# Kernel optimization log

Hardware: AMD Instinct MI355X
Metric: run time of the kernel (lower is better)

## Reference

```python
import jax, jax.numpy as jnp
import numpy as np

DIM = 128          # per-head dim P (== feature dim of x, y)
HEADS = 8
INNER = DIM * HEADS  # 1024
HIDDEN = int(DIM * 4.0)  # 512
EPS = 1e-5
LS_INIT = 1e-5


def _ln(x, w, b):
    mu = jnp.mean(x, axis=-1, keepdims=True)
    var = jnp.var(x, axis=-1, keepdims=True)
    return (x - mu) * jax.lax.rsqrt(var + EPS) * w + b


def setup_inputs() -> dict:
    key = jax.random.key(0)
    ks = jax.random.split(key, 10)
    B, N, M = 8, 1024, 1024
    s_in = 1.0 / np.sqrt(DIM)
    s_inner = 1.0 / np.sqrt(INNER)
    s_hid = 1.0 / np.sqrt(HIDDEN)
    return {
        "x": jax.random.normal(ks[0], (B, N, DIM), jnp.float32),
        "y": jax.random.normal(ks[1], (B, M, DIM), jnp.float32),
        "norm_x_w": jnp.ones((DIM,), jnp.float32),
        "norm_x_b": jnp.zeros((DIM,), jnp.float32),
        "norm_y_w": jnp.ones((DIM,), jnp.float32),
        "norm_y_b": jnp.zeros((DIM,), jnp.float32),
        "q_w": jax.random.uniform(ks[2], (INNER, DIM), jnp.float32, -s_in, s_in),
        "kv_w": jax.random.uniform(ks[3], (2 * INNER, DIM), jnp.float32, -s_in, s_in),
        "proj_w": jax.random.uniform(ks[4], (DIM, INNER), jnp.float32, -s_inner, s_inner),
        "proj_b": jax.random.uniform(ks[5], (DIM,), jnp.float32, -s_inner, s_inner),
        "ls1_gamma": jnp.full((DIM,), LS_INIT, jnp.float32),
        "norm_out_w": jnp.ones((DIM,), jnp.float32),
        "norm_out_b": jnp.zeros((DIM,), jnp.float32),
        "fc1_w": jax.random.uniform(ks[6], (HIDDEN, DIM), jnp.float32, -s_in, s_in),
        "fc1_b": jax.random.uniform(ks[7], (HIDDEN,), jnp.float32, -s_in, s_in),
        "fc2_w": jax.random.uniform(ks[8], (DIM, HIDDEN), jnp.float32, -s_hid, s_hid),
        "fc2_b": jax.random.uniform(ks[9], (DIM,), jnp.float32, -s_hid, s_hid),
        "ls2_gamma": jnp.full((DIM,), LS_INIT, jnp.float32),
    }


def reference(x, y, norm_x_w, norm_x_b, norm_y_w, norm_y_b, q_w, kv_w,
              proj_w, proj_b, ls1_gamma, norm_out_w, norm_out_b,
              fc1_w, fc1_b, fc2_w, fc2_b, ls2_gamma):
    B, N, P = x.shape
    M = y.shape[1]
    scale = P ** (-0.5)

    xn = _ln(x, norm_x_w, norm_x_b)
    yn = _ln(y, norm_y_w, norm_y_b)

    # q: (B,N,H,P) -> bhnp ; kv: (B,M,2,H,P)
    q = (xn @ q_w.T).reshape(B, N, HEADS, P).transpose(0, 2, 1, 3)
    kv = (yn @ kv_w.T).reshape(B, M, 2, HEADS, P)
    k = kv[:, :, 0].transpose(0, 2, 1, 3)  # bhmp
    v = kv[:, :, 1].transpose(0, 2, 1, 3)  # bhmp

    attn = jnp.einsum('bhnp,bhmp->bhnm', q, k) * scale
    attn = jax.nn.softmax(attn, axis=-1)
    o = jnp.einsum('bhnm,bhmp->bhnp', attn, v)
    o = o.transpose(0, 2, 1, 3).reshape(B, N, INNER)
    o = o @ proj_w.T + proj_b
    x = x + o * ls1_gamma

    h = _ln(x, norm_out_w, norm_out_b)
    h = jax.nn.relu(h @ fc1_w.T + fc1_b)
    h = h @ fc2_w.T + fc2_b
    x = x + h * ls2_gamma
    return x
```

## Files before the change

kernel.cpp:

```cpp
#include <hip/hip_runtime.h>
#include <stdint.h>

#define DIM    128
#define HEADS  8
#define INNER  1024
#define HIDDEN 512
#define BATCH  8
#define SEQ    1024
#define ROWS   8192

typedef __attribute__((ext_vector_type(8))) short bf16x8;
typedef __attribute__((ext_vector_type(4))) float f32x4;
typedef __attribute__((ext_vector_type(4))) unsigned short u16x4;

#define QSCALE (0.08838834764831845f * 1.4426950408889634f)

#define AS1 __attribute__((address_space(1)))
#define AS3 __attribute__((address_space(3)))

static __device__ __forceinline__ float b2f(unsigned short u) {
    union { float f; unsigned int i; } v; v.i = ((unsigned int)u) << 16; return v.f;
}
static __device__ __forceinline__ unsigned short f2b(float f) {
    union { float f; unsigned int i; } v; v.f = f;
    unsigned int x = v.i;
    return (unsigned short)((x + 0x7fffu + ((x >> 16) & 1u)) >> 16);
}
static __device__ __forceinline__ unsigned int cvt_pk_bf16(float a, float b) {
    unsigned int r;
    asm("v_cvt_pk_bf16_f32 %0, %1, %2" : "=v"(r) : "v"(a), "v"(b));
    return r;
}
static __device__ __forceinline__ void gl_lds16(const unsigned short* g, unsigned short* l) {
    __builtin_amdgcn_global_load_lds((AS1 void*)g, (AS3 void*)l, 16, 0, 0);
}

static __device__ __forceinline__ size_t pa_idx(int row, int k, int K) {
    return ((size_t)((row >> 4) * (K >> 5) + (k >> 5)) << 9)
         + (size_t)(((((k >> 3) & 3) << 4) + (row & 15)) << 3) + (size_t)(k & 7);
}

template<int K>
static __device__ __forceinline__ void cvtw(const float* __restrict__ W,
                                            unsigned short* __restrict__ Wp, int j)
{
    const int c  = j & 15;
    const int gw = (j >> 4) & 3;
    const int blk = j >> 6;
    const int ks = blk & ((K >> 5) - 1);
    const int nt = blk / (K >> 5);
    const int n  = nt * 16 + c;
    const int kb = ks * 32 + gw * 8;
    const float4 a = *(const float4*)(W + (size_t)n * K + kb);
    const float4 b = *(const float4*)(W + (size_t)n * K + kb + 4);
    u16x4 o0, o1;
    o0[0] = f2b(a.x); o0[1] = f2b(a.y); o0[2] = f2b(a.z); o0[3] = f2b(a.w);
    o1[0] = f2b(b.x); o1[1] = f2b(b.y); o1[2] = f2b(b.z); o1[3] = f2b(b.w);
    *(u16x4*)(Wp + (size_t)j * 8)     = o0;
    *(u16x4*)(Wp + (size_t)j * 8 + 4) = o1;
}

__global__ __launch_bounds__(256)
void cvt_all_kernel(const float* __restrict__ s0, unsigned short* __restrict__ d0,
                    const float* __restrict__ s1, unsigned short* __restrict__ d1,
                    const float* __restrict__ s2, unsigned short* __restrict__ d2,
                    const float* __restrict__ s3, unsigned short* __restrict__ d3,
                    const float* __restrict__ s4, unsigned short* __restrict__ d4)
{
    int j = blockIdx.x * 256 + threadIdx.x;
    if (j < 16384)                 { cvtw<128>(s0, d0, j);  return; }
    if ((j -= 16384) < 32768)      { cvtw<128>(s1, d1, j);  return; }
    if ((j -= 32768) < 16384)      { cvtw<1024>(s2, d2, j); return; }
    if ((j -= 16384) < 8192)       { cvtw<128>(s3, d3, j);  return; }
    j -= 8192;                       cvtw<512>(s4, d4, j);
}

static __device__ __forceinline__ void ln_row(const float* __restrict__ in,
                                              const float* __restrict__ w,
                                              const float* __restrict__ b,
                                              unsigned short* __restrict__ out,
                                              int row, int lane)
{
    const float2 xv = *(const float2*)(in + (size_t)row*DIM + lane*2);
    float x0 = xv.x, x1 = xv.y;
    float s = x0 + x1;
    float q = x0*x0 + x1*x1;
    #pragma unroll
    for (int off = 32; off > 0; off >>= 1) {
        s += __shfl_xor(s, off);
        q += __shfl_xor(q, off);
    }
    const float mu  = s * (1.0f/128.0f);
    const float var = q * (1.0f/128.0f) - mu*mu;
    const float rs  = rsqrtf(var + 1e-5f);
    const float2 wv = *(const float2*)(w + lane*2);
    const float2 bv = *(const float2*)(b + lane*2);
    unsigned short o0 = f2b((x0 - mu) * rs * wv.x + bv.x);
    unsigned short o1 = f2b((x1 - mu) * rs * wv.y + bv.y);
    *(unsigned int*)(out + pa_idx(row, lane*2, 128)) = (unsigned int)o0 | ((unsigned int)o1 << 16);
}

__global__ __launch_bounds__(256)
void ln_dual_kernel(const float* __restrict__ inx, const float* __restrict__ wx,
                    const float* __restrict__ bx, unsigned short* __restrict__ outx,
                    const float* __restrict__ iny, const float* __restrict__ wy,
                    const float* __restrict__ by, unsigned short* __restrict__ outy)
{
    const int row  = blockIdx.x * 4 + (threadIdx.x >> 6);
    const int lane = threadIdx.x & 63;
    if (blockIdx.y == 0) ln_row(inx, wx, bx, outx, row, lane);
    else                 ln_row(iny, wy, by, outy, row, lane);
}

__global__ __launch_bounds__(256)
void qkv_kernel(const unsigned short* __restrict__ xn,
                const unsigned short* __restrict__ yn,
                const unsigned short* __restrict__ wq,
                const unsigned short* __restrict__ wkv,
                unsigned short* __restrict__ qb,
                unsigned short* __restrict__ kpm,
                unsigned short* __restrict__ vpm)
{
    const int lane = threadIdx.x & 63;
    const int wave = threadIdx.x >> 6;
    const int g    = lane >> 4;
    const int c16  = lane & 15;
    const int bx   = blockIdx.x;
    const int by   = blockIdx.y;

    f32x4 acc[4];
    #pragma unroll
    for (int t = 0; t < 4; ++t) acc[t] = (f32x4){0.f, 0.f, 0.f, 0.f};

    if (bx < 32) {
        const bool isq = bx < 16;
        const unsigned short* W = isq ? wq : wkv;
        const unsigned short* Aact = isq ? xn : yn;
        const int wt = (bx & 15) * 4 + wave;
        #pragma unroll
        for (int ks = 0; ks < 4; ++ks) {
            bf16x8 wf = *(const bf16x8*)(W + (((size_t)(wt*4 + ks)) << 9) + lane*8);
            #pragma unroll
            for (int t = 0; t < 4; ++t) {
                bf16x8 af = *(const bf16x8*)(Aact + (((size_t)((by*4 + t)*4 + ks)) << 9) + lane*8);
                acc[t] = __builtin_amdgcn_mfma_f32_16x16x32_bf16(wf, af, acc[t], 0, 0, 0);
            }
        }
        const int n_w0 = (bx & 15)*64 + wave*16 + g*4;
        const int hh = n_w0 >> 7;
        const int p0 = n_w0 & 127;
        #pragma unroll
        for (int t = 0; t < 4; ++t) {
            const int m_row = by*64 + t*16 + c16;
            const int bb = m_row >> 10, m = m_row & 1023;
            u16x4 o;
            if (isq) {
                o[0] = f2b(acc[t][0]*QSCALE); o[1] = f2b(acc[t][1]*QSCALE);
                o[2] = f2b(acc[t][2]*QSCALE); o[3] = f2b(acc[t][3]*QSCALE);
                *(u16x4*)&qb[(((size_t)(bb*HEADS + hh))*SEQ + m)*DIM + p0] = o;
            } else {
                o[0] = f2b(acc[t][0]); o[1] = f2b(acc[t][1]);
                o[2] = f2b(acc[t][2]); o[3] = f2b(acc[t][3]);
                const int chunk = m >> 5, sl = (m >> 4) & 1, cl = m & 15;
                const int ksl = p0 >> 5, gl = (p0 >> 3) & 3, el0 = p0 & 7;
                *(u16x4*)&kpm[(size_t)(bb*HEADS + hh)*SEQ*DIM
                    + (size_t)((chunk*8 + sl*4 + ksl)*64 + gl*16 + cl)*8 + el0] = o;
            }
        }
    } else {
        const int mt = by*4 + wave;
        #pragma unroll
        for (int ks = 0; ks < 4; ++ks) {
            bf16x8 af = *(const bf16x8*)(yn + (((size_t)(mt*4 + ks)) << 9) + lane*8);
            #pragma unroll
            for (int t = 0; t < 4; ++t) {
                const int nt = 64 + (bx - 32)*4 + t;
                bf16x8 wf = *(const bf16x8*)(wkv + (((size_t)(nt*4 + ks)) << 9) + lane*8);
                acc[t] = __builtin_amdgcn_mfma_f32_16x16x32_bf16(af, wf, acc[t], 0, 0, 0);
            }
        }
        const int m_row0 = by*64 + wave*16 + g*4;
        const int bb = m_row0 >> 10;
        const int m0 = m_row0 & 1023;
        const int chunk = m0 >> 5, gl = (m0 >> 3) & 3, el0 = m0 & 7;
        #pragma unroll
        for (int t = 0; t < 4; ++t) {
            const int p = (bx - 32)*64 + t*16 + c16;
            const int hh = p >> 7, pp = p & 127, pcl = pp >> 4, cl = pp & 15;
            u16x4 o;
            o[0] = f2b(acc[t][0]); o[1] = f2b(acc[t][1]);
            o[2] = f2b(acc[t][2]); o[3] = f2b(acc[t][3]);
            *(u16x4*)&vpm[(size_t)(bb*HEADS + hh)*SEQ*DIM
                + (size_t)((chunk*8 + pcl)*64 + gl*16 + cl)*8 + el0] = o;
        }
    }
}

__global__ __launch_bounds__(512)
void attn_kernel(const unsigned short* __restrict__ qbuf,
                 const unsigned short* __restrict__ kperm,
                 const unsigned short* __restrict__ vperm,
                 unsigned short* __restrict__ obuf)
{
    __shared__ unsigned short kbuf[2][8192];
    __shared__ unsigned short vbuf[2][8192];
    __shared__ unsigned short pls[8][640];

    const int lane = threadIdx.x & 63;
    const int wave = threadIdx.x >> 6;
    const int g    = lane >> 4;
    const int c16  = lane & 15;

    const int j    = blockIdx.x;
    const int bh   = (j & 7) * 8 + (j >> 6);
    const int nblk = (j >> 3) & 7;
    const int n0   = nblk * 128 + wave * 16;
    const int bb   = bh >> 3, hh = bh & 7;

    const unsigned short* Q  = qbuf  + (size_t)bh * SEQ * DIM;
    const unsigned short* Kb = kperm + (size_t)bh * SEQ * DIM;
    const unsigned short* Vb = vperm + (size_t)bh * SEQ * DIM;

    #pragma unroll
    for (int i = 0; i < 4; ++i) {
        gl_lds16(Kb + (wave*4 + i)*512 + lane*8, &kbuf[0][(wave*4 + i)*512]);
        gl_lds16(Vb + (wave*4 + i)*512 + lane*8, &vbuf[0][(wave*4 + i)*512]);
    }

    bf16x8 qf[4];
    #pragma unroll
    for (int ks = 0; ks < 4; ++ks)
        qf[ks] = *(const bf16x8*)(Q + (size_t)(n0 + c16)*DIM + ks*32 + g*8);

    f32x4 oacc[8];
    #pragma unroll
    for (int pc = 0; pc < 8; ++pc) oacc[pc] = (f32x4){0.f,0.f,0.f,0.f};
    float mi = 8.0f;
    float li0 = 0.f, li1 = 0.f;

    __syncthreads();

    int cur = 0;
    for (int ip = 0; ip < 16; ++ip, cur ^= 1) {
        if (ip != 15) {
            const unsigned short* Ks = Kb + (size_t)(ip + 1) * 8192;
            const unsigned short* Vs = Vb + (size_t)(ip + 1) * 8192;
            #pragma unroll
            for (int i = 0; i < 4; ++i) {
                gl_lds16(Ks + (wave*4 + i)*512 + lane*8, &kbuf[cur ^ 1][(wave*4 + i)*512]);
                gl_lds16(Vs + (wave*4 + i)*512 + lane*8, &vbuf[cur ^ 1][(wave*4 + i)*512]);
            }
        }

        f32x4 st[4];
        #pragma unroll
        for (int c = 0; c < 2; ++c)
            #pragma unroll
            for (int s = 0; s < 2; ++s) {
                f32x4 a = (f32x4){0.f,0.f,0.f,0.f};
                #pragma unroll
                for (int ks = 0; ks < 4; ++ks) {
                    bf16x8 kf = *(const bf16x8*)&kbuf[cur][c*4096 + (s*4 + ks)*512 + lane*8];
                    a = __builtin_amdgcn_mfma_f32_16x16x32_bf16(kf, qf[ks], a, 0, 0, 0);
                }
                st[c*2 + s] = a;
            }

        #pragma unroll
        for (int c = 0; c < 2; ++c) {
            bf16x8 vf[8];
            #pragma unroll
            for (int pc = 0; pc < 8; ++pc)
                vf[pc] = *(const bf16x8*)&vbuf[cur][c*4096 + (pc*64 + lane)*8];

            const f32x4 sa = st[c*2 + 0];
            const f32x4 sb = st[c*2 + 1];
            float cmax = fmaxf(fmaxf(fmaxf(sa[0], sa[1]), fmaxf(sa[2], sa[3])),
                               fmaxf(fmaxf(sb[0], sb[1]), fmaxf(sb[2], sb[3])));

            if (!__all(cmax - mi <= 8.0f)) {
                float rmax = cmax;
                rmax = fmaxf(rmax, __shfl_xor(rmax, 16));
                rmax = fmaxf(rmax, __shfl_xor(rmax, 32));
                const float mnew  = fmaxf(mi, rmax);
                const float alpha = exp2f(mi - mnew);
                mi = mnew;
                li0 *= alpha; li1 *= alpha;
                float ar[4];
                #pragma unroll
                for (int r = 0; r < 4; ++r) ar[r] = __shfl(alpha, g*4 + r);
                #pragma unroll
                for (int pc = 0; pc < 8; ++pc)
                    #pragma unroll
                    for (int r = 0; r < 4; ++r) oacc[pc][r] *= ar[r];
            }

            uint2 pw[2];
            {
                float p0 = exp2f(sa[0] - mi), p1 = exp2f(sa[1] - mi);
                float p2 = exp2f(sa[2] - mi), p3 = exp2f(sa[3] - mi);
                float p4 = exp2f(sb[0] - mi), p5 = exp2f(sb[1] - mi);
                float p6 = exp2f(sb[2] - mi), p7 = exp2f(sb[3] - mi);
                li0 += (p0 + p1) + (p2 + p3);
                li1 += (p4 + p5) + (p6 + p7);
                pw[0].x = cvt_pk_bf16(p0, p1); pw[0].y = cvt_pk_bf16(p2, p3);
                pw[1].x = cvt_pk_bf16(p4, p5); pw[1].y = cvt_pk_bf16(p6, p7);
            }

            unsigned short* pbase = &pls[wave][0];
            *(uint2*)(pbase + c16*40 + 0*16 + g*4) = pw[0];
            *(uint2*)(pbase + c16*40 + 1*16 + g*4) = pw[1];

            bf16x8 pa = *(const bf16x8*)(pbase + c16*40 + g*8);
            #pragma unroll
            for (int pc = 0; pc < 8; ++pc)
                oacc[pc] = __builtin_amdgcn_mfma_f32_16x16x32_bf16(pa, vf[pc], oacc[pc], 0, 0, 0);
        }

        __syncthreads();
    }

    float li = li0 + li1;
    li += __shfl_xor(li, 16);
    li += __shfl_xor(li, 32);
    float lr[4];
    #pragma unroll
    for (int r = 0; r < 4; ++r) lr[r] = 1.f / __shfl(li, g*4 + r);
    #pragma unroll
    for (int pc = 0; pc < 8; ++pc)
        #pragma unroll
        for (int r = 0; r < 4; ++r) {
            const int row = bb*SEQ + n0 + g*4 + r;
            const int k   = hh*DIM + pc*16 + c16;
            obuf[pa_idx(row, k, INNER)] = f2b(oacc[pc][r] * lr[r]);
        }
}

__global__ __launch_bounds__(256)
void projln_kernel(const unsigned short* __restrict__ A,
                   const unsigned short* __restrict__ W,
                   const float* __restrict__ bias,
                   const float* __restrict__ gamma,
                   const float* __restrict__ xres,
                   float* __restrict__ x1,
                   const float* __restrict__ lnw, const float* __restrict__ lnb,
                   unsigned short* __restrict__ hin)
{
    __shared__ float part[4][16][2];

    const int lane = threadIdx.x & 63;
    const int wave = threadIdx.x >> 6;
    const int g    = lane >> 4;
    const int c16  = lane & 15;
    const int mt   = blockIdx.x;

    f32x4 acc[2];
    acc[0] = (f32x4){0.f,0.f,0.f,0.f};
    acc[1] = (f32x4){0.f,0.f,0.f,0.f};

    #pragma unroll 4
    for (int ks = 0; ks < 32; ++ks) {
        bf16x8 af = *(const bf16x8*)(A + (((size_t)(mt*32 + ks)) << 9) + lane*8);
        #pragma unroll
        for (int t = 0; t < 2; ++t) {
            bf16x8 wf = *(const bf16x8*)(W + (((size_t)((wave*2 + t)*32 + ks)) << 9) + lane*8);
            acc[t] = __builtin_amdgcn_mfma_f32_16x16x32_bf16(af, wf, acc[t], 0, 0, 0);
        }
    }

    float v[2][4];
    #pragma unroll
    for (int t = 0; t < 2; ++t) {
        const int col = wave*32 + t*16 + c16;
        const float bb = bias[col], gg = gamma[col];
        #pragma unroll
        for (int r = 0; r < 4; ++r) {
            const int row = mt*16 + g*4 + r;
            const float xv = xres[(size_t)row*DIM + col];
            v[t][r] = xv + (acc[t][r] + bb) * gg;
            x1[(size_t)row*DIM + col] = v[t][r];
        }
    }
    #pragma unroll
    for (int r = 0; r < 4; ++r) {
        float s = v[0][r] + v[1][r];
        float q = v[0][r]*v[0][r] + v[1][r]*v[1][r];
        #pragma unroll
        for (int off = 1; off < 16; off <<= 1) {
            s += __shfl_xor(s, off);
            q += __shfl_xor(q, off);
        }
        if (c16 == 0) { part[wave][g*4+r][0] = s; part[wave][g*4+r][1] = q; }
    }
    __syncthreads();

    #pragma unroll
    for (int r = 0; r < 4; ++r) {
        const int lr = g*4 + r;
        const float s = part[0][lr][0] + part[1][lr][0] + part[2][lr][0] + part[3][lr][0];
        const float q = part[0][lr][1] + part[1][lr][1] + part[2][lr][1] + part[3][lr][1];
        const float mu  = s * (1.0f/128.0f);
        const float var = q * (1.0f/128.0f) - mu*mu;
        const float rs  = rsqrtf(var + 1e-5f);
        const int row = mt*16 + lr;
        #pragma unroll
        for (int t = 0; t < 2; ++t) {
            const int col = wave*32 + t*16 + c16;
            const float hv = (v[t][r] - mu) * rs * lnw[col] + lnb[col];
            hin[pa_idx(row, col, 128)] = f2b(hv);
        }
    }
}

__global__ __launch_bounds__(256)
void fc_kernel(const unsigned short* __restrict__ hin,
               const unsigned short* __restrict__ W1,
               const float* __restrict__ b1,
               const unsigned short* __restrict__ W2,
               const float* __restrict__ b2,
               const float* __restrict__ gamma2,
               const float* __restrict__ x1,
               float* __restrict__ dout)
{
    __shared__ unsigned short h[16][520];

    const int lane = threadIdx.x & 63;
    const int wave = threadIdx.x >> 6;
    const int g    = lane >> 4;
    const int c16  = lane & 15;
    const int mt   = blockIdx.x;

    f32x4 a1[8];
    #pragma unroll
    for (int t = 0; t < 8; ++t) a1[t] = (f32x4){0.f,0.f,0.f,0.f};
    #pragma unroll
    for (int ks = 0; ks < 4; ++ks) {
        bf16x8 af = *(const bf16x8*)(hin + (((size_t)(mt*4 + ks)) << 9) + lane*8);
        #pragma unroll
        for (int t = 0; t < 8; ++t) {
            const int nt = wave*8 + t;
            bf16x8 wf = *(const bf16x8*)(W1 + (((size_t)(nt*4 + ks)) << 9) + lane*8);
            a1[t] = __builtin_amdgcn_mfma_f32_16x16x32_bf16(af, wf, a1[t], 0, 0, 0);
        }
    }
    #pragma unroll
    for (int t = 0; t < 8; ++t) {
        const int col = wave*128 + t*16 + c16;
        const float bb = b1[col];
        #pragma unroll
        for (int r = 0; r < 4; ++r)
            h[g*4 + r][col] = f2b(fmaxf(a1[t][r] + bb, 0.f));
    }
    __syncthreads();

    f32x4 a2[2];
    a2[0] = (f32x4){0.f,0.f,0.f,0.f};
    a2[1] = (f32x4){0.f,0.f,0.f,0.f};
    #pragma unroll 4
    for (int ks = 0; ks < 16; ++ks) {
        bf16x8 af = *(const bf16x8*)&h[c16][ks*32 + g*8];
        #pragma unroll
        for (int t = 0; t < 2; ++t) {
            const int nt = wave*2 + t;
            bf16x8 wf = *(const bf16x8*)(W2 + (((size_t)(nt*16 + ks)) << 9) + lane*8);
            a2[t] = __builtin_amdgcn_mfma_f32_16x16x32_bf16(af, wf, a2[t], 0, 0, 0);
        }
    }
    #pragma unroll
    for (int t = 0; t < 2; ++t) {
        const int col = wave*32 + t*16 + c16;
        const float bb = b2[col], gg = gamma2[col];
        #pragma unroll
        for (int r = 0; r < 4; ++r) {
            const int row = mt*16 + g*4 + r;
            dout[(size_t)row*DIM + col] = x1[(size_t)row*DIM + col] + (a2[t][r] + bb) * gg;
        }
    }
}

extern "C" void kernel_launch(void* const* d_in, const int* in_sizes, int n_in,
                              void* d_out, int out_size, void* d_ws, size_t ws_size,
                              hipStream_t stream)
{
    const float* x         = (const float*)d_in[0];
    const float* y         = (const float*)d_in[1];
    const float* norm_x_w  = (const float*)d_in[2];
    const float* norm_x_b  = (const float*)d_in[3];
    const float* norm_y_w  = (const float*)d_in[4];
    const float* norm_y_b  = (const float*)d_in[5];
    const float* q_w       = (const float*)d_in[6];
    const float* kv_w      = (const float*)d_in[7];
    const float* proj_w    = (const float*)d_in[8];
    const float* proj_b    = (const float*)d_in[9];
    const float* ls1_gamma = (const float*)d_in[10];
    const float* norm_o_w  = (const float*)d_in[11];
    const float* norm_o_b  = (const float*)d_in[12];
    const float* fc1_w     = (const float*)d_in[13];
    const float* fc1_b     = (const float*)d_in[14];
    const float* fc2_w     = (const float*)d_in[15];
    const float* fc2_b     = (const float*)d_in[16];
    const float* ls2_gamma = (const float*)d_in[17];

    char* ws = (char*)d_ws;
    size_t off = 0;
    auto alloc = [&](size_t bytes) {
        void* p = ws + off;
        off += (bytes + 255) & ~(size_t)255;
        return p;
    };
    unsigned short* xn  = (unsigned short*)alloc((size_t)ROWS*DIM*2);
    unsigned short* yn  = (unsigned short*)alloc((size_t)ROWS*DIM*2);
    unsigned short* qb  = (unsigned short*)alloc((size_t)ROWS*INNER*2);
    unsigned short* kpm = (unsigned short*)alloc((size_t)ROWS*INNER*2);
    unsigned short* vpm = (unsigned short*)alloc((size_t)ROWS*INNER*2);
    unsigned short* ob  = (unsigned short*)alloc((size_t)ROWS*INNER*2);
    float*          x1  = (float*)alloc((size_t)ROWS*DIM*4);
    unsigned short* hin = (unsigned short*)alloc((size_t)ROWS*DIM*2);
    unsigned short* wq   = (unsigned short*)alloc((size_t)INNER*DIM*2);
    unsigned short* wkv  = (unsigned short*)alloc((size_t)2*INNER*DIM*2);
    unsigned short* wpr  = (unsigned short*)alloc((size_t)DIM*INNER*2);
    unsigned short* wf1  = (unsigned short*)alloc((size_t)HIDDEN*DIM*2);
    unsigned short* wf2  = (unsigned short*)alloc((size_t)DIM*HIDDEN*2);

    cvt_all_kernel<<<dim3(320), 256, 0, stream>>>(
        q_w, wq, kv_w, wkv, proj_w, wpr, fc1_w, wf1, fc2_w, wf2);

    ln_dual_kernel<<<dim3(ROWS/4, 2), 256, 0, stream>>>(
        x, norm_x_w, norm_x_b, xn, y, norm_y_w, norm_y_b, yn);

    qkv_kernel<<<dim3(48, ROWS/64), 256, 0, stream>>>(xn, yn, wq, wkv, qb, kpm, vpm);

    attn_kernel<<<dim3(512), 512, 0, stream>>>(qb, kpm, vpm, ob);

    projln_kernel<<<dim3(ROWS/16), 256, 0, stream>>>(
        ob, wpr, proj_b, ls1_gamma, x, x1, norm_o_w, norm_o_b, hin);

    fc_kernel<<<dim3(ROWS/16), 256, 0, stream>>>(
        hin, wf1, fc1_b, wf2, fc2_b, ls2_gamma, x1, (float*)d_out);
}
```

Baseline: 112.6 us.

## Switch attention to 32x32x16 MFMA tiles with register-shuffled P operand

The attention kernel now uses 32x32x16 bf16 MFMA instead of 16x16x32. It runs 4 waves per block, each owning 32 query rows, and processes 32 keys per iteration. The K/V permuted layouts written by the QKV kernel are rearranged to match the new operand fragments. The softmax probabilities are rearranged into the PV A-operand with cross-half lane shuffles rather than a round trip through LDS, which removes the per-wave P scratch buffer. The cost is more iterations with a block-wide barrier each, and more accumulator registers per wave.

```diff
diff --git a/kernel.cpp b/kernel.cpp
--- a/kernel.cpp
+++ b/kernel.cpp
@@ -11,6 +11,7 @@
 
 typedef __attribute__((ext_vector_type(8))) short bf16x8;
 typedef __attribute__((ext_vector_type(4))) float f32x4;
+typedef __attribute__((ext_vector_type(16))) float f32x16;
 typedef __attribute__((ext_vector_type(4))) unsigned short u16x4;
 
 #define QSCALE (0.08838834764831845f * 1.4426950408889634f)
@@ -161,10 +162,10 @@
             } else {
                 o[0] = f2b(acc[t][0]); o[1] = f2b(acc[t][1]);
                 o[2] = f2b(acc[t][2]); o[3] = f2b(acc[t][3]);
-                const int chunk = m >> 5, sl = (m >> 4) & 1, cl = m & 15;
-                const int ksl = p0 >> 5, gl = (p0 >> 3) & 3, el0 = p0 & 7;
+                const int chunk = m >> 5;
+                const int ds = p0 >> 4, dhi = (p0 >> 3) & 1, de = p0 & 7;
                 *(u16x4*)&kpm[(size_t)(bb*HEADS + hh)*SEQ*DIM
-                    + (size_t)((chunk*8 + sl*4 + ksl)*64 + gl*16 + cl)*8 + el0] = o;
+                    + (size_t)(chunk*4096 + ds*512 + dhi*256 + (m & 31)*8 + de)] = o;
             }
         }
     } else {
@@ -182,39 +183,38 @@
         const int m_row0 = by*64 + wave*16 + g*4;
         const int bb = m_row0 >> 10;
         const int m0 = m_row0 & 1023;
-        const int chunk = m0 >> 5, gl = (m0 >> 3) & 3, el0 = m0 & 7;
+        const int chunk = m0 >> 5, s = (m0 >> 4) & 1, mhi = (m0 >> 3) & 1, e0 = m0 & 7;
         #pragma unroll
         for (int t = 0; t < 4; ++t) {
             const int p = (bx - 32)*64 + t*16 + c16;
-            const int hh = p >> 7, pp = p & 127, pcl = pp >> 4, cl = pp & 15;
+            const int hh = p >> 7, pp = p & 127, pt = pp >> 5, pc = pp & 31;
             u16x4 o;
             o[0] = f2b(acc[t][0]); o[1] = f2b(acc[t][1]);
             o[2] = f2b(acc[t][2]); o[3] = f2b(acc[t][3]);
             *(u16x4*)&vpm[(size_t)(bb*HEADS + hh)*SEQ*DIM
-                + (size_t)((chunk*8 + pcl)*64 + gl*16 + cl)*8 + el0] = o;
-        }
-    }
-}
-
-__global__ __launch_bounds__(512)
+                + (size_t)(chunk*4096 + (pt*2 + s)*512 + mhi*256 + pc*8 + e0)] = o;
+        }
+    }
+}
+
+__global__ __launch_bounds__(256)
 void attn_kernel(const unsigned short* __restrict__ qbuf,
                  const unsigned short* __restrict__ kperm,
                  const unsigned short* __restrict__ vperm,
                  unsigned short* __restrict__ obuf)
 {
-    __shared__ unsigned short kbuf[2][8192];
-    __shared__ unsigned short vbuf[2][8192];
-    __shared__ unsigned short pls[8][640];
+    __shared__ unsigned short kbuf[2][4096];
+    __shared__ unsigned short vbuf[2][4096];
 
     const int lane = threadIdx.x & 63;
     const int wave = threadIdx.x >> 6;
-    const int g    = lane >> 4;
-    const int c16  = lane & 15;
+    const int l31  = lane & 31;
+    const int hi   = lane >> 5;
 
     const int j    = blockIdx.x;
     const int bh   = (j & 7) * 8 + (j >> 6);
     const int nblk = (j >> 3) & 7;
-    const int n0   = nblk * 128 + wave * 16;
+    const int n0   = nblk * 128 + wave * 32;
     const int bb   = bh >> 3, hh = bh & 7;
 
     const unsigned short* Q  = qbuf  + (size_t)bh * SEQ * DIM;
@@ -222,117 +222,125 @@
     const unsigned short* Vb = vperm + (size_t)bh * SEQ * DIM;
 
     #pragma unroll
-    for (int i = 0; i < 4; ++i) {
-        gl_lds16(Kb + (wave*4 + i)*512 + lane*8, &kbuf[0][(wave*4 + i)*512]);
-        gl_lds16(Vb + (wave*4 + i)*512 + lane*8, &vbuf[0][(wave*4 + i)*512]);
-    }
-
-    bf16x8 qf[4];
-    #pragma unroll
-    for (int ks = 0; ks < 4; ++ks)
-        qf[ks] = *(const bf16x8*)(Q + (size_t)(n0 + c16)*DIM + ks*32 + g*8);
-
-    f32x4 oacc[8];
-    #pragma unroll
-    for (int pc = 0; pc < 8; ++pc) oacc[pc] = (f32x4){0.f,0.f,0.f,0.f};
+    for (int i = 0; i < 2; ++i) {
+        gl_lds16(Kb + (wave*2 + i)*512 + lane*8, &kbuf[0][(wave*2 + i)*512]);
+        gl_lds16(Vb + (wave*2 + i)*512 + lane*8, &vbuf[0][(wave*2 + i)*512]);
+    }
+
+    bf16x8 qf[8];
+    #pragma unroll
+    for (int ds = 0; ds < 8; ++ds)
+        qf[ds] = *(const bf16x8*)(Q + (size_t)(n0 + l31)*DIM + ds*16 + hi*8);
+
+    f32x16 oacc[4];
+    #pragma unroll
+    for (int pt = 0; pt < 4; ++pt)
+        #pragma unroll
+        for (int r = 0; r < 16; ++r) oacc[pt][r] = 0.f;
     float mi = 8.0f;
     float li0 = 0.f, li1 = 0.f;
 
     __syncthreads();
 
     int cur = 0;
-    for (int ip = 0; ip < 16; ++ip, cur ^= 1) {
-        if (ip != 15) {
-            const unsigned short* Ks = Kb + (size_t)(ip + 1) * 8192;
-            const unsigned short* Vs = Vb + (size_t)(ip + 1) * 8192;
+    for (int it = 0; it < 32; ++it, cur ^= 1) {
+        if (it != 31) {
+            const unsigned short* Ks = Kb + (size_t)(it + 1) * 4096;
+            const unsigned short* Vs = Vb + (size_t)(it + 1) * 4096;
             #pragma unroll
-            for (int i = 0; i < 4; ++i) {
-                gl_lds16(Ks + (wave*4 + i)*512 + lane*8, &kbuf[cur ^ 1][(wave*4 + i)*512]);
-                gl_lds16(Vs + (wave*4 + i)*512 + lane*8, &vbuf[cur ^ 1][(wave*4 + i)*512]);
+            for (int i = 0; i < 2; ++i) {
+                gl_lds16(Ks + (wave*2 + i)*512 + lane*8, &kbuf[cur ^ 1][(wave*2 + i)*512]);
+                gl_lds16(Vs + (wave*2 + i)*512 + lane*8, &vbuf[cur ^ 1][(wave*2 + i)*512]);
             }
         }
 
-        f32x4 st[4];
-        #pragma unroll
-        for (int c = 0; c < 2; ++c)
+        f32x16 st;
+        #pragma unroll
+        for (int r = 0; r < 16; ++r) st[r] = 0.f;
+        #pragma unroll
+        for (int ds = 0; ds < 8; ++ds) {
+            bf16x8 kf = *(const bf16x8*)&kbuf[cur][ds*512 + lane*8];
+            st = __builtin_amdgcn_mfma_f32_32x32x16_bf16(kf, qf[ds], st, 0, 0, 0);
+        }
+
+        bf16x8 vf[8];
+        #pragma unroll
+        for (int f = 0; f < 8; ++f)
+            vf[f] = *(const bf16x8*)&vbuf[cur][f*512 + lane*8];
+
+        float cmax = st[0];
+        #pragma unroll
+        for (int r = 1; r < 16; ++r) cmax = fmaxf(cmax, st[r]);
+
+        if (!__all(cmax - mi <= 8.0f)) {
+            float rmax = fmaxf(cmax, __shfl_xor(cmax, 32));
+            const float mnew  = fmaxf(mi, rmax);
+            const float alpha = exp2f(mi - mnew);
+            mi = mnew;
+            li0 *= alpha; li1 *= alpha;
+            float ar[16];
             #pragma unroll
-            for (int s = 0; s < 2; ++s) {
-                f32x4 a = (f32x4){0.f,0.f,0.f,0.f};
+            for (int r = 0; r < 16; ++r)
+                ar[r] = __shfl(alpha, (r & 3) + 8*(r >> 2) + 4*hi);
+            #pragma unroll
+            for (int pt = 0; pt < 4; ++pt)
                 #pragma unroll
-                for (int ks = 0; ks < 4; ++ks) {
-                    bf16x8 kf = *(const bf16x8*)&kbuf[cur][c*4096 + (s*4 + ks)*512 + lane*8];
-                    a = __builtin_amdgcn_mfma_f32_16x16x32_bf16(kf, qf[ks], a, 0, 0, 0);
-                }
-                st[c*2 + s] = a;
-            }
-
-        #pragma unroll
-        for (int c = 0; c < 2; ++c) {
-            bf16x8 vf[8];
-            #pragma unroll
-            for (int pc = 0; pc < 8; ++pc)
-                vf[pc] = *(const bf16x8*)&vbuf[cur][c*4096 + (pc*64 + lane)*8];
-
-            const f32x4 sa = st[c*2 + 0];
-            const f32x4 sb = st[c*2 + 1];
-            float cmax = fmaxf(fmaxf(fmaxf(sa[0], sa[1]), fmaxf(sa[2], sa[3])),
-                               fmaxf(fmaxf(sb[0], sb[1]), fmaxf(sb[2], sb[3])));
-
-            if (!__all(cmax - mi <= 8.0f)) {
-                float rmax = cmax;
-                rmax = fmaxf(rmax, __shfl_xor(rmax, 16));
-                rmax = fmaxf(rmax, __shfl_xor(rmax, 32));
-                const float mnew  = fmaxf(mi, rmax);
-                const float alpha = exp2f(mi - mnew);
-                mi = mnew;
-                li0 *= alpha; li1 *= alpha;
-                float ar[4];
-                #pragma unroll
-                for (int r = 0; r < 4; ++r) ar[r] = __shfl(alpha, g*4 + r);
-                #pragma unroll
-                for (int pc = 0; pc < 8; ++pc)
-                    #pragma unroll
-                    for (int r = 0; r < 4; ++r) oacc[pc][r] *= ar[r];
-            }
-
-            uint2 pw[2];
-            {
-                float p0 = exp2f(sa[0] - mi), p1 = exp2f(sa[1] - mi);
-                float p2 = exp2f(sa[2] - mi), p3 = exp2f(sa[3] - mi);
-                float p4 = exp2f(sb[0] - mi), p5 = exp2f(sb[1] - mi);
-                float p6 = exp2f(sb[2] - mi), p7 = exp2f(sb[3] - mi);
-                li0 += (p0 + p1) + (p2 + p3);
-                li1 += (p4 + p5) + (p6 + p7);
-                pw[0].x = cvt_pk_bf16(p0, p1); pw[0].y = cvt_pk_bf16(p2, p3);
-                pw[1].x = cvt_pk_bf16(p4, p5); pw[1].y = cvt_pk_bf16(p6, p7);
-            }
-
-            unsigned short* pbase = &pls[wave][0];
-            *(uint2*)(pbase + c16*40 + 0*16 + g*4) = pw[0];
-            *(uint2*)(pbase + c16*40 + 1*16 + g*4) = pw[1];
-
-            bf16x8 pa = *(const bf16x8*)(pbase + c16*40 + g*8);
-            #pragma unroll
-            for (int pc = 0; pc < 8; ++pc)
-                oacc[pc] = __builtin_amdgcn_mfma_f32_16x16x32_bf16(pa, vf[pc], oacc[pc], 0, 0, 0);
+                for (int r = 0; r < 16; ++r) oacc[pt][r] *= ar[r];
+        }
+
+        float p[16];
+        #pragma unroll
+        for (int r = 0; r < 16; ++r) p[r] = exp2f(st[r] - mi);
+        li0 += ((p[0]+p[1]) + (p[2]+p[3])) + ((p[4]+p[5]) + (p[6]+p[7]));
+        li1 += ((p[8]+p[9]) + (p[10]+p[11])) + ((p[12]+p[13]) + (p[14]+p[15]));
+
+        union { unsigned w[4]; bf16x8 v; } pa0, pa1;
+        {
+            unsigned a0 = cvt_pk_bf16(p[0], p[1]),  a1 = cvt_pk_bf16(p[2], p[3]);
+            unsigned b0 = cvt_pk_bf16(p[4], p[5]),  b1 = cvt_pk_bf16(p[6], p[7]);
+            unsigned sa0 = __shfl_xor((int)a0, 32), sb0 = __shfl_xor((int)b0, 32);
+            unsigned sa1 = __shfl_xor((int)a1, 32), sb1 = __shfl_xor((int)b1, 32);
+            pa0.w[0] = hi ? sb0 : a0;
+            pa0.w[1] = hi ? sb1 : a1;
+            pa0.w[2] = hi ? b0  : sa0;
+            pa0.w[3] = hi ? b1  : sa1;
+        }
+        {
+            unsigned a0 = cvt_pk_bf16(p[8], p[9]),   a1 = cvt_pk_bf16(p[10], p[11]);
+            unsigned b0 = cvt_pk_bf16(p[12], p[13]), b1 = cvt_pk_bf16(p[14], p[15]);
+            unsigned sa0 = __shfl_xor((int)a0, 32), sb0 = __shfl_xor((int)b0, 32);
+            unsigned sa1 = __shfl_xor((int)a1, 32), sb1 = __shfl_xor((int)b1, 32);
+            pa1.w[0] = hi ? sb0 : a0;
+            pa1.w[1] = hi ? sb1 : a1;
+            pa1.w[2] = hi ? b0  : sa0;
+            pa1.w[3] = hi ? b1  : sa1;
+        }
+
+        #pragma unroll
+        for (int pt = 0; pt < 4; ++pt) {
+            oacc[pt] = __builtin_amdgcn_mfma_f32_32x32x16_bf16(pa0.v, vf[pt*2 + 0], oacc[pt], 0, 0, 0);
+            oacc[pt] = __builtin_amdgcn_mfma_f32_32x32x16_bf16(pa1.v, vf[pt*2 + 1], oacc[pt], 0, 0, 0);
         }
 
         __syncthreads();
     }
 
     float li = li0 + li1;
-    li += __shfl_xor(li, 16);
     li += __shfl_xor(li, 32);
-    float lr[4];
-    #pragma unroll
-    for (int r = 0; r < 4; ++r) lr[r] = 1.f / __shfl(li, g*4 + r);
-    #pragma unroll
-    for (int pc = 0; pc < 8; ++pc)
-        #pragma unroll
-        for (int r = 0; r < 4; ++r) {
-            const int row = bb*SEQ + n0 + g*4 + r;
-            const int k   = hh*DIM + pc*16 + c16;
-            obuf[pa_idx(row, k, INNER)] = f2b(oacc[pc][r] * lr[r]);
+    const float inv = 1.f / li;
+    float lrv[16];
+    #pragma unroll
+    for (int r = 0; r < 16; ++r)
+        lrv[r] = __shfl(inv, (r & 3) + 8*(r >> 2) + 4*hi);
+
+    #pragma unroll
+    for (int pt = 0; pt < 4; ++pt)
+        #pragma unroll
+        for (int r = 0; r < 16; ++r) {
+            const int qr  = (r & 3) + 8*(r >> 2) + 4*hi;
+            const int row = bb*SEQ + n0 + qr;
+            const int k   = hh*DIM + pt*32 + l31;
+            obuf[pa_idx(row, k, INNER)] = f2b(oacc[pt][r] * lrv[r]);
         }
 }
 
@@ -530,7 +538,7 @@
 
     qkv_kernel<<<dim3(48, ROWS/64), 256, 0, stream>>>(xn, yn, wq, wkv, qb, kpm, vpm);
 
-    attn_kernel<<<dim3(512), 512, 0, stream>>>(qb, kpm, vpm, ob);
+    attn_kernel<<<dim3(512), 256, 0, stream>>>(qb, kpm, vpm, ob);
 
     projln_kernel<<<dim3(ROWS/16), 256, 0, stream>>>(
         ob, wpr, proj_b, ls1_gamma, x, x1, norm_o_w, norm_o_b, hin);
```

Measured after the change: 148.7 us. +32.1%, slower.
